# Kernel optimization log

Hardware: AMD Instinct MI355X
Metric: run time of the kernel (lower is better)

## Reference

```python
import jax, jax.numpy as jnp
import numpy as np

B, T, D = 1, 2048, 2048
H, HD = 16, 128          # n_heads, head_dim
RD = 64                  # rotary_emb_dim
K = 4                    # short conv kernel size
EPS = 1e-5


def setup_inputs() -> dict:
    key = jax.random.key(0)
    ks = jax.random.split(key, 10)
    hidden_states = jax.random.normal(ks[0], (B, T, D), dtype=jnp.float32)
    # standard RoPE tables for the rotary sub-dimension
    inv_freq = 1.0 / (10000.0 ** (jnp.arange(0, RD, 2, dtype=jnp.float32) / RD))  # [RD/2]
    pos = jnp.arange(T, dtype=jnp.float32)
    freqs = pos[:, None] * inv_freq[None, :]          # [T, RD/2]
    emb = jnp.concatenate([freqs, freqs], axis=-1)    # [T, RD]
    cos = jnp.broadcast_to(jnp.cos(emb)[None], (B, T, RD))
    sin = jnp.broadcast_to(jnp.sin(emb)[None], (B, T, RD))
    s = 1.0 / np.sqrt(D)
    return {
        "hidden_states": hidden_states,
        "cos": cos, "sin": sin,
        "Wq": jax.random.normal(ks[1], (D, D), jnp.float32) * s,
        "Wk": jax.random.normal(ks[2], (D, D), jnp.float32) * s,
        "Wv": jax.random.normal(ks[3], (D, D), jnp.float32) * s,
        "Wo": jax.random.normal(ks[4], (D, D), jnp.float32) * s,
        "conv_q_w": jax.random.normal(ks[5], (D, K), jnp.float32) * 0.5,
        "conv_k_w": jax.random.normal(ks[6], (D, K), jnp.float32) * 0.5,
        "conv_v_w": jax.random.normal(ks[7], (D, K), jnp.float32) * 0.5,
        "q_norm_w": jnp.ones((HD,), jnp.float32),
        "k_norm_w": jnp.ones((HD,), jnp.float32),
    }


def _causal_conv_silu(x, w):
    # x: [B,T,D], w: [D,K]; depthwise causal conv (tap K-1 hits current pos) + SiLU
    xp = jnp.pad(x, ((0, 0), (K - 1, 0), (0, 0)))
    y = sum(xp[:, j:j + T, :] * w[None, None, :, j] for j in range(K))
    return jax.nn.silu(y)


def _rms_norm(x, w):
    # x: [..., HD]
    var = jnp.mean(x * x, axis=-1, keepdims=True)
    return x * jax.lax.rsqrt(var + EPS) * w


def _rotate_half(x):
    x1, x2 = x[..., : x.shape[-1] // 2], x[..., x.shape[-1] // 2:]
    return jnp.concatenate([-x2, x1], axis=-1)


def _apply_rope(x, cos, sin):
    # x: [B,H,T,HD]; cos/sin: [B,T,RD] -> unsqueeze head dim; partial rotary branch
    cos = cos[:, None, :, :]
    sin = sin[:, None, :, :]
    x_rot, x_pass = x[..., :RD], x[..., RD:]
    x_rot = x_rot * cos + _rotate_half(x_rot) * sin
    # faithful to source: negates rotated part when rotary_dim != head_dim
    return jnp.concatenate([-x_rot, x_pass], axis=-1)


def reference(hidden_states, cos, sin, Wq, Wk, Wv, Wo,
              conv_q_w, conv_k_w, conv_v_w, q_norm_w, k_norm_w):
    # projections (Linear with bias=False: y = x @ W^T)
    q = hidden_states @ Wq.T
    k = hidden_states @ Wk.T
    v = hidden_states @ Wv.T
    # short causal depthwise conv + SiLU
    q = _causal_conv_silu(q, conv_q_w)
    k = _causal_conv_silu(k, conv_k_w)
    v = _causal_conv_silu(v, conv_v_w)
    # split heads: [B,T,D] -> [B,T,H,HD]
    q = q.reshape(B, T, H, HD)
    k = k.reshape(B, T, H, HD)
    v = v.reshape(B, T, H, HD)
    # per-head RMSNorm, then [B,H,T,HD]
    q = _rms_norm(q, q_norm_w).transpose(0, 2, 1, 3)
    k = _rms_norm(k, k_norm_w).transpose(0, 2, 1, 3)
    v = v.transpose(0, 2, 1, 3)
    # RoPE (partial)
    q = _apply_rope(q, cos, sin)
    k = _apply_rope(k, cos, sin)
    # causal attention
    scale = 1.0 / np.sqrt(HD)
    scores = jnp.einsum('bhqd,bhkd->bhqk', q, k) * scale
    causal = jnp.tril(jnp.ones((T, T), dtype=bool))
    scores = jnp.where(causal[None, None], scores, jnp.float32(-1e30))
    probs = jax.nn.softmax(scores, axis=-1)
    attn = jnp.einsum('bhqk,bhkd->bhqd', probs, v)
    # [B,H,T,HD] -> [B,T,D], output projection
    out = attn.transpose(0, 2, 1, 3).reshape(B, T, D) @ Wo.T
    return out
```

## Files before the change

### kernel.cpp

```cpp
#include <hip/hip_runtime.h>
#include <hip/hip_bf16.h>

#define T_SEQ 2048
#define D_MODEL 2048
#define NH 16
#define HDIM 128
#define RD_ROT 64

typedef __bf16 bf16x8 __attribute__((ext_vector_type(8)));
typedef float f32x4 __attribute__((ext_vector_type(4)));

__device__ __forceinline__ void async_copy16(const __bf16* g, __bf16* l) {
    __builtin_amdgcn_global_load_lds(
        (const __attribute__((address_space(1))) void*)g,
        (__attribute__((address_space(3))) void*)l, 16, 0, 0);
}

__global__ __launch_bounds__(256) void cast_kernel(
    const float* __restrict__ s0, const float* __restrict__ s1, const float* __restrict__ s2,
    const float* __restrict__ s3, const float* __restrict__ s4,
    __bf16* __restrict__ d0, __bf16* __restrict__ d1, __bf16* __restrict__ d2,
    __bf16* __restrict__ d3, __bf16* __restrict__ d4)
{
    const float* s; __bf16* d;
    switch (blockIdx.y) {
        case 0: s = s0; d = d0; break;
        case 1: s = s1; d = d1; break;
        case 2: s = s2; d = d2; break;
        case 3: s = s3; d = d3; break;
        default: s = s4; d = d4; break;
    }
    size_t base = (size_t)blockIdx.x * D_MODEL + (size_t)threadIdx.x * 8;
    f32x4 a = *(const f32x4*)(s + base);
    f32x4 b = *(const f32x4*)(s + base + 4);
    bf16x8 o;
    #pragma unroll
    for (int i = 0; i < 4; i++) { o[i] = (__bf16)a[i]; o[i + 4] = (__bf16)b[i]; }
    *(bf16x8*)(d + base) = o;
}

__global__ __launch_bounds__(256) void gemm_bt_kernel(
    const __bf16* __restrict__ A,
    const __bf16* __restrict__ B0, const __bf16* __restrict__ B1, const __bf16* __restrict__ B2,
    __bf16* __restrict__ C0, __bf16* __restrict__ C1, __bf16* __restrict__ C2)
{
    constexpr int BM = 128, BK = 32, KD = D_MODEL;
    const __bf16* Bm = blockIdx.z == 0 ? B0 : (blockIdx.z == 1 ? B1 : B2);
    __bf16* Cm       = blockIdx.z == 0 ? C0 : (blockIdx.z == 1 ? C1 : C2);

    __shared__ __align__(16) __bf16 As[BM * BK];
    __shared__ __align__(16) __bf16 Bs[BM * BK];

    const int lane = threadIdx.x & 63;
    const int wave = threadIdx.x >> 6;
    const int r15  = lane & 15;
    const int quad = lane >> 4;
    const int bm = blockIdx.x * BM;
    const int bn = blockIdx.y * BM;
    const int wm = (wave >> 1) * 64;
    const int wn = (wave & 1) * 64;

    f32x4 acc[4][4] = {};

    const int srow = wave * 32 + (lane >> 2);
    const int sg   = (lane & 3) ^ ((lane >> 2) & 3);

    for (int k0 = 0; k0 < KD; k0 += BK) {
        async_copy16(A  + (size_t)(bm + srow)      * KD + k0 + sg * 8, &As[wave * 1024]);
        async_copy16(A  + (size_t)(bm + srow + 16) * KD + k0 + sg * 8, &As[wave * 1024 + 512]);
        async_copy16(Bm + (size_t)(bn + srow)      * KD + k0 + sg * 8, &Bs[wave * 1024]);
        async_copy16(Bm + (size_t)(bn + srow + 16) * KD + k0 + sg * 8, &Bs[wave * 1024 + 512]);
        __syncthreads();

        bf16x8 av[4], bv[4];
        #pragma unroll
        for (int mt = 0; mt < 4; mt++)
            av[mt] = *(const bf16x8*)&As[(wm + mt * 16 + r15) * 32 + ((quad ^ (r15 & 3)) << 3)];
        #pragma unroll
        for (int nt = 0; nt < 4; nt++)
            bv[nt] = *(const bf16x8*)&Bs[(wn + nt * 16 + r15) * 32 + ((quad ^ (r15 & 3)) << 3)];
        #pragma unroll
        for (int mt = 0; mt < 4; mt++)
            #pragma unroll
            for (int nt = 0; nt < 4; nt++)
                acc[mt][nt] = __builtin_amdgcn_mfma_f32_16x16x32_bf16(av[mt], bv[nt], acc[mt][nt], 0, 0, 0);
        __syncthreads();
    }

    #pragma unroll
    for (int mt = 0; mt < 4; mt++) {
        #pragma unroll
        for (int r = 0; r < 4; r++) {
            size_t row = bm + wm + mt * 16 + quad * 4 + r;
            #pragma unroll
            for (int nt = 0; nt < 4; nt++) {
                size_t col = bn + wn + nt * 16 + r15;
                Cm[row * D_MODEL + col] = (__bf16)acc[mt][nt][r];
            }
        }
    }
}

__global__ __launch_bounds__(256) void gemm_bt_splitk_kernel(
    const __bf16* __restrict__ A, const __bf16* __restrict__ Bm, float* __restrict__ C)
{
    constexpr int BM = 128, BK = 32, KD = D_MODEL;
    __shared__ __align__(16) __bf16 As[BM * BK];
    __shared__ __align__(16) __bf16 Bs[BM * BK];

    const int lane = threadIdx.x & 63;
    const int wave = threadIdx.x >> 6;
    const int r15  = lane & 15;
    const int quad = lane >> 4;
    const int bm = blockIdx.x * BM;
    const int bn = blockIdx.y * BM;
    const int wm = (wave >> 1) * 64;
    const int wn = (wave & 1) * 64;
    const int kbase = blockIdx.z * (KD / 2);

    f32x4 acc[4][4] = {};
    const int srow = wave * 32 + (lane >> 2);
    const int sg   = (lane & 3) ^ ((lane >> 2) & 3);

    for (int k0 = kbase; k0 < kbase + KD / 2; k0 += BK) {
        async_copy16(A  + (size_t)(bm + srow)      * KD + k0 + sg * 8, &As[wave * 1024]);
        async_copy16(A  + (size_t)(bm + srow + 16) * KD + k0 + sg * 8, &As[wave * 1024 + 512]);
        async_copy16(Bm + (size_t)(bn + srow)      * KD + k0 + sg * 8, &Bs[wave * 1024]);
        async_copy16(Bm + (size_t)(bn + srow + 16) * KD + k0 + sg * 8, &Bs[wave * 1024 + 512]);
        __syncthreads();

        bf16x8 av[4], bv[4];
        #pragma unroll
        for (int mt = 0; mt < 4; mt++)
            av[mt] = *(const bf16x8*)&As[(wm + mt * 16 + r15) * 32 + ((quad ^ (r15 & 3)) << 3)];
        #pragma unroll
        for (int nt = 0; nt < 4; nt++)
            bv[nt] = *(const bf16x8*)&Bs[(wn + nt * 16 + r15) * 32 + ((quad ^ (r15 & 3)) << 3)];
        #pragma unroll
        for (int mt = 0; mt < 4; mt++)
            #pragma unroll
            for (int nt = 0; nt < 4; nt++)
                acc[mt][nt] = __builtin_amdgcn_mfma_f32_16x16x32_bf16(av[mt], bv[nt], acc[mt][nt], 0, 0, 0);
        __syncthreads();
    }

    #pragma unroll
    for (int mt = 0; mt < 4; mt++) {
        #pragma unroll
        for (int r = 0; r < 4; r++) {
            size_t row = bm + wm + mt * 16 + quad * 4 + r;
            #pragma unroll
            for (int nt = 0; nt < 4; nt++) {
                size_t col = bn + wn + nt * 16 + r15;
                atomicAdd(&C[row * D_MODEL + col], acc[mt][nt][r]);
            }
        }
    }
}

__global__ __launch_bounds__(256) void preproc_qk_kernel(
    const __bf16* __restrict__ q_raw, const __bf16* __restrict__ k_raw,
    const float* __restrict__ cwq, const float* __restrict__ cwk,
    const float* __restrict__ qnw, const float* __restrict__ knw,
    const float* __restrict__ cosb, const float* __restrict__ sinb,
    __bf16* __restrict__ q_proc, __bf16* __restrict__ k_proc)
{
    const int t = blockIdx.x;
    const int which = blockIdx.y;
    const __bf16* X = which ? k_raw : q_raw;
    const float*  W = which ? cwk : cwq;
    const float*  nw = which ? knw : qnw;
    __bf16* P = which ? k_proc : q_proc;
    const float SC = which ? 1.0f : 0.08838834764831845f;

    const int tid = threadIdx.x;
    const int c0  = tid * 8;
    const int h   = tid >> 4;
    const int dl0 = (tid & 15) * 8;

    f32x4 wv[8];
    #pragma unroll
    for (int i = 0; i < 8; i++) wv[i] = *(const f32x4*)&W[(c0 + i) * 4];

    float acc[8] = {};
    #pragma unroll
    for (int j = 0; j < 4; j++) {
        int tt = t + j - 3;
        if (tt >= 0) {
            bf16x8 xv = *(const bf16x8*)&X[(size_t)tt * D_MODEL + c0];
            #pragma unroll
            for (int i = 0; i < 8; i++) acc[i] += (float)xv[i] * wv[i][j];
        }
    }
    float sil[8], ss = 0.f;
    #pragma unroll
    for (int i = 0; i < 8; i++) {
        float s = acc[i] / (1.f + __expf(-acc[i]));
        sil[i] = s; ss += s * s;
    }
    #pragma unroll
    for (int off = 1; off < 16; off <<= 1) ss += __shfl_xor(ss, off);
    float inv = rsqrtf(ss * (1.f / 128.f) + 1e-5f);

    f32x4 nv0 = *(const f32x4*)&nw[dl0];
    f32x4 nv1 = *(const f32x4*)&nw[dl0 + 4];
    float yn[8];
    #pragma unroll
    for (int i = 0; i < 8; i++) yn[i] = sil[i] * inv * (i < 4 ? nv0[i] : nv1[i - 4]);

    float partner[8];
    #pragma unroll
    for (int i = 0; i < 8; i++) partner[i] = __shfl_xor(yn[i], 4);

    bf16x8 o;
    if (dl0 < RD_ROT) {
        f32x4 cv0 = *(const f32x4*)&cosb[t * RD_ROT + dl0];
        f32x4 cv1 = *(const f32x4*)&cosb[t * RD_ROT + dl0 + 4];
        f32x4 sv0 = *(const f32x4*)&sinb[t * RD_ROT + dl0];
        f32x4 sv1 = *(const f32x4*)&sinb[t * RD_ROT + dl0 + 4];
        #pragma unroll
        for (int i = 0; i < 8; i++) {
            int dl = dl0 + i;
            float c = i < 4 ? cv0[i] : cv1[i - 4];
            float s = i < 4 ? sv0[i] : sv1[i - 4];
            float rot = (dl < 32) ? -partner[i] : partner[i];
            o[i] = (__bf16)((yn[i] * c + rot * s) * SC);
        }
    } else {
        #pragma unroll
        for (int i = 0; i < 8; i++) o[i] = (__bf16)(yn[i] * SC);
    }
    *(bf16x8*)&P[((size_t)h * T_SEQ + t) * HDIM + dl0] = o;
}

__global__ __launch_bounds__(128) void preproc_v_kernel(
    const __bf16* __restrict__ v_raw, const float* __restrict__ cwv,
    __bf16* __restrict__ v_t)
{
    const int t0 = blockIdx.x * 8;
    const int h = blockIdx.y;
    const int dl = threadIdx.x;
    const int d = h * HDIM + dl;

    f32x4 wv = *(const f32x4*)&cwv[d * 4];
    float x[11];
    #pragma unroll
    for (int m = 0; m < 11; m++) {
        int tt = t0 - 3 + m;
        x[m] = (tt >= 0) ? (float)v_raw[(size_t)tt * D_MODEL + d] : 0.f;
    }
    bf16x8 o;
    #pragma unroll
    for (int r = 0; r < 8; r++) {
        float y = x[r] * wv[0] + x[r + 1] * wv[1] + x[r + 2] * wv[2] + x[r + 3] * wv[3];
        o[r] = (__bf16)(y / (1.f + __expf(-y)));
    }
    *(bf16x8*)&v_t[((size_t)h * HDIM + dl) * T_SEQ + t0] = o;
}

__global__ __launch_bounds__(256, 2) void attn_kernel(
    const __bf16* __restrict__ Qp,
    const __bf16* __restrict__ Kp,
    const __bf16* __restrict__ Vt,
    __bf16* __restrict__ Op)
{
    constexpr int TK = 64, PSTR = 72;
    __shared__ __align__(16) __bf16 Ks[2][TK * HDIM];
    __shared__ __align__(16) __bf16 Vs[2][HDIM * TK];
    __shared__ __align__(16) __bf16 Ps[64 * PSTR];

    const int lane = threadIdx.x & 63;
    const int wave = threadIdx.x >> 6;
    const int r15  = lane & 15;
    const int quad = lane >> 4;
    const int h = blockIdx.y;
    const int qi = (blockIdx.y & 8) ? ((int)gridDim.x - 1 - (int)blockIdx.x) : (int)blockIdx.x;
    const int q0 = qi * TK;

    const __bf16* Kb = Kp + (size_t)h * T_SEQ * HDIM;
    const __bf16* Vb = Vt + (size_t)h * HDIM * T_SEQ;

    const int kchunk = wave * 4;
    const int krow_l = (lane >> 4);
    const int kg     = lane & 15;
    const int vrow_l = (lane >> 3);
    const int vg     = lane & 7;

    bf16x8 qf[4];
    const __bf16* qbase = Qp + ((size_t)h * T_SEQ + q0 + wave * 16 + r15) * HDIM;
    #pragma unroll
    for (int s = 0; s < 4; s++) qf[s] = *(const bf16x8*)(qbase + s * 32 + quad * 8);

    f32x4 oacc[8] = {};
    float mrow[4], lsum[4];
    #pragma unroll
    for (int r = 0; r < 4; r++) { mrow[r] = -1e30f; lsum[r] = 0.f; }

    const int ntk = qi + 1;

    #pragma unroll
    for (int i = 0; i < 4; i++) {
        int ck = kchunk + i;
        int krow = ck * 4 + krow_l;
        int vrow = ck * 8 + vrow_l;
        async_copy16(Kb + (size_t)krow * HDIM + (kg ^ (krow & 15)) * 8, &Ks[0][ck * 512]);
        async_copy16(Vb + (size_t)vrow * T_SEQ + (vg ^ (vrow & 7)) * 8, &Vs[0][ck * 512]);
    }

    for (int it = 0; it < ntk; it++) {
        const int buf = it & 1;
        const bool last = (it == ntk - 1);
        __syncthreads();

        if (!last) {
            const int tkn = (it + 1) * TK;
            const int nbuf = buf ^ 1;
            #pragma unroll
            for (int i = 0; i < 4; i++) {
                int ck = kchunk + i;
                int krow = ck * 4 + krow_l;
                int vrow = ck * 8 + vrow_l;
                async_copy16(Kb + (size_t)(tkn + krow) * HDIM + (kg ^ (krow & 15)) * 8, &Ks[nbuf][ck * 512]);
                async_copy16(Vb + (size_t)vrow * T_SEQ + tkn + (vg ^ (vrow & 7)) * 8, &Vs[nbuf][ck * 512]);
            }
        }

        f32x4 sacc[4] = {};
        #pragma unroll
        for (int s = 0; s < 4; s++) {
            #pragma unroll
            for (int nt = 0; nt < 4; nt++) {
                bf16x8 kf = *(const bf16x8*)&Ks[buf][(nt * 16 + r15) * HDIM + (((s * 4 + quad) ^ r15) << 3)];
                sacc[nt] = __builtin_amdgcn_mfma_f32_16x16x32_bf16(qf[s], kf, sacc[nt], 0, 0, 0);
            }
        }

        float alpha[4];
        #pragma unroll
        for (int r = 0; r < 4; r++) {
            if (last) {
                int qrow = q0 + wave * 16 + quad * 4 + r;
                #pragma unroll
                for (int nt = 0; nt < 4; nt++) {
                    int kcol = it * TK + nt * 16 + r15;
                    if (kcol > qrow) sacc[nt][r] = -1e30f;
                }
            }
            float tm = fmaxf(fmaxf(sacc[0][r], sacc[1][r]), fmaxf(sacc[2][r], sacc[3][r]));
            #pragma unroll
            for (int off = 1; off < 16; off <<= 1) tm = fmaxf(tm, __shfl_xor(tm, off));
            float mn = fmaxf(mrow[r], tm);
            float a = __expf(mrow[r] - mn);
            mrow[r] = mn;
            alpha[r] = a;
            float ps = 0.f;
            #pragma unroll
            for (int nt = 0; nt < 4; nt++) {
                float p = __expf(sacc[nt][r] - mn);
                sacc[nt][r] = p;
                ps += p;
            }
            lsum[r] = lsum[r] * a + ps;
        }
        #pragma unroll
        for (int nt = 0; nt < 8; nt++)
            #pragma unroll
            for (int r = 0; r < 4; r++) oacc[nt][r] *= alpha[r];

        #pragma unroll
        for (int nt = 0; nt < 4; nt++)
            #pragma unroll
            for (int r = 0; r < 4; r++)
                Ps[(wave * 16 + quad * 4 + r) * PSTR + nt * 16 + r15] = (__bf16)sacc[nt][r];

        #pragma unroll
        for (int s2 = 0; s2 < 2; s2++) {
            bf16x8 pf = *(const bf16x8*)&Ps[(wave * 16 + r15) * PSTR + s2 * 32 + quad * 8];
            #pragma unroll
            for (int nt = 0; nt < 8; nt++) {
                bf16x8 vf = *(const bf16x8*)&Vs[buf][(nt * 16 + r15) * TK + (((s2 * 4 + quad) ^ (r15 & 7)) << 3)];
                oacc[nt] = __builtin_amdgcn_mfma_f32_16x16x32_bf16(pf, vf, oacc[nt], 0, 0, 0);
            }
        }
    }

    #pragma unroll
    for (int r = 0; r < 4; r++) {
        float l = lsum[r];
        #pragma unroll
        for (int off = 1; off < 16; off <<= 1) l += __shfl_xor(l, off);
        float inv = 1.0f / l;
        size_t row = q0 + wave * 16 + quad * 4 + r;
        #pragma unroll
        for (int nt = 0; nt < 8; nt++)
            Op[row * D_MODEL + h * HDIM + nt * 16 + r15] = (__bf16)(oacc[nt][r] * inv);
    }
}

extern "C" void kernel_launch(void* const* d_in, const int* in_sizes, int n_in,
                              void* d_out, int out_size, void* d_ws, size_t ws_size,
                              hipStream_t stream) {
    (void)in_sizes; (void)n_in; (void)out_size; (void)ws_size;
    const float* hidden = (const float*)d_in[0];
    const float* cosb   = (const float*)d_in[1];
    const float* sinb   = (const float*)d_in[2];
    const float* Wq     = (const float*)d_in[3];
    const float* Wk     = (const float*)d_in[4];
    const float* Wv     = (const float*)d_in[5];
    const float* Wo     = (const float*)d_in[6];
    const float* cwq    = (const float*)d_in[7];
    const float* cwk    = (const float*)d_in[8];
    const float* cwv    = (const float*)d_in[9];
    const float* qnw    = (const float*)d_in[10];
    const float* knw    = (const float*)d_in[11];

    const size_t NEL = (size_t)T_SEQ * D_MODEL;
    __bf16* ws = (__bf16*)d_ws;
    __bf16* h_bf   = ws + 0 * NEL;
    __bf16* Wq_bf  = ws + 1 * NEL;
    __bf16* Wk_bf  = ws + 2 * NEL;
    __bf16* Wv_bf  = ws + 3 * NEL;
    __bf16* Wo_bf  = ws + 4 * NEL;
    __bf16* q_raw  = ws + 5 * NEL;
    __bf16* k_raw  = ws + 6 * NEL;
    __bf16* v_raw  = ws + 7 * NEL;
    __bf16* q_proc = Wq_bf;
    __bf16* k_proc = Wk_bf;
    __bf16* v_t    = Wv_bf;
    __bf16* attn_b = h_bf;
    float*  out    = (float*)d_out;

    cast_kernel<<<dim3(T_SEQ, 5), 256, 0, stream>>>(hidden, Wq, Wk, Wv, Wo,
                                                    h_bf, Wq_bf, Wk_bf, Wv_bf, Wo_bf);
    gemm_bt_kernel<<<dim3(16, 16, 3), 256, 0, stream>>>(
        h_bf, Wq_bf, Wk_bf, Wv_bf, q_raw, k_raw, v_raw);
    preproc_qk_kernel<<<dim3(T_SEQ, 2), 256, 0, stream>>>(
        q_raw, k_raw, cwq, cwk, qnw, knw, cosb, sinb, q_proc, k_proc);
    preproc_v_kernel<<<dim3(T_SEQ / 8, NH), 128, 0, stream>>>(v_raw, cwv, v_t);
    attn_kernel<<<dim3(T_SEQ / 64, NH), 256, 0, stream>>>(q_proc, k_proc, v_t, attn_b);
    hipMemsetAsync(d_out, 0, NEL * sizeof(float), stream);
    gemm_bt_splitk_kernel<<<dim3(16, 16, 2), 256, 0, stream>>>(attn_b, Wo_bf, out);
}
```

Baseline: 345.2 us.

## Rework attention to 32x32 MFMA with split-K waves and max-free softmax

Result: slower. 354.8 us (+2.8%).

```diff
diff --git a/kernel.cpp b/kernel.cpp
--- a/kernel.cpp
+++ b/kernel.cpp
@@ -9,6 +9,7 @@
 
 typedef __bf16 bf16x8 __attribute__((ext_vector_type(8)));
 typedef float f32x4 __attribute__((ext_vector_type(4)));
+typedef float f32x16 __attribute__((ext_vector_type(16)));
 
 __device__ __forceinline__ void async_copy16(const __bf16* g, __bf16* l) {
     __builtin_amdgcn_global_load_lds(
@@ -264,37 +265,42 @@
     const __bf16* __restrict__ Vt,
     __bf16* __restrict__ Op)
 {
-    constexpr int TK = 64, PSTR = 72;
+    constexpr int TK = 64;
     __shared__ __align__(16) __bf16 Ks[2][TK * HDIM];
     __shared__ __align__(16) __bf16 Vs[2][HDIM * TK];
-    __shared__ __align__(16) __bf16 Ps[64 * PSTR];
+    __shared__ __align__(16) __bf16 Ps[4][32 * 64];
+    float* Omrg = (float*)Ks;
+    float* Lmrg = (float*)Ps;
 
     const int lane = threadIdx.x & 63;
     const int wave = threadIdx.x >> 6;
-    const int r15  = lane & 15;
-    const int quad = lane >> 4;
+    const int rowg = wave >> 1;
+    const int par  = wave & 1;
+    const int c31  = lane & 31;
+    const int h5   = lane >> 5;
     const int h = blockIdx.y;
     const int qi = (blockIdx.y & 8) ? ((int)gridDim.x - 1 - (int)blockIdx.x) : (int)blockIdx.x;
-    const int q0 = qi * TK;
+    const int q0 = qi * 64;
+    const int rw = q0 + rowg * 32;
 
     const __bf16* Kb = Kp + (size_t)h * T_SEQ * HDIM;
     const __bf16* Vb = Vt + (size_t)h * HDIM * T_SEQ;
 
+    bf16x8 qf[8];
+    {
+        const __bf16* qb = Qp + ((size_t)h * T_SEQ + rw + c31) * HDIM + h5 * 8;
+        #pragma unroll
+        for (int kc = 0; kc < 8; kc++) qf[kc] = *(const bf16x8*)(qb + kc * 16);
+    }
+
     const int kchunk = wave * 4;
-    const int krow_l = (lane >> 4);
+    const int krow_l = lane >> 4;
     const int kg     = lane & 15;
-    const int vrow_l = (lane >> 3);
+    const int vrow_l = lane >> 3;
     const int vg     = lane & 7;
 
-    bf16x8 qf[4];
-    const __bf16* qbase = Qp + ((size_t)h * T_SEQ + q0 + wave * 16 + r15) * HDIM;
-    #pragma unroll
-    for (int s = 0; s < 4; s++) qf[s] = *(const bf16x8*)(qbase + s * 32 + quad * 8);
-
-    f32x4 oacc[8] = {};
-    float mrow[4], lsum[4];
-    #pragma unroll
-    for (int r = 0; r < 4; r++) { mrow[r] = -1e30f; lsum[r] = 0.f; }
+    f32x16 oacc[4] = {};
+    float lsum[16] = {};
 
     const int ntk = qi + 1;
 
@@ -309,10 +315,9 @@
 
     for (int it = 0; it < ntk; it++) {
         const int buf = it & 1;
-        const bool last = (it == ntk - 1);
         __syncthreads();
 
-        if (!last) {
+        if (it + 1 < ntk) {
             const int tkn = (it + 1) * TK;
             const int nbuf = buf ^ 1;
             #pragma unroll
@@ -325,75 +330,99 @@
             }
         }
 
-        f32x4 sacc[4] = {};
-        #pragma unroll
-        for (int s = 0; s < 4; s++) {
+        if ((it & 1) != par) continue;
+        const bool diag = (it == qi);
+        const int ntmax = (diag && rowg == 0) ? 1 : 2;
+
+        f32x16 sacc[2] = {};
+        #pragma unroll
+        for (int nt = 0; nt < 2; nt++) {
+            if (nt >= ntmax) break;
+            #pragma unroll
+            for (int kc = 0; kc < 8; kc++) {
+                int row = nt * 32 + c31;
+                int g = kc * 2 + h5;
+                bf16x8 kf = *(const bf16x8*)&Ks[buf][row * HDIM + ((g ^ (row & 15)) << 3)];
+                sacc[nt] = __builtin_amdgcn_mfma_f32_32x32x16_bf16(qf[kc], kf, sacc[nt], 0, 0, 0);
+            }
+        }
+
+        #pragma unroll
+        for (int nt = 0; nt < 2; nt++) {
+            if (nt >= ntmax) break;
+            const bool dmask = diag && (nt == rowg);
+            int col = it * TK + nt * 32 + c31;
+            #pragma unroll
+            for (int reg = 0; reg < 16; reg++) {
+                int row = rw + (reg & 3) + 8 * (reg >> 2) + 4 * h5;
+                float p = __expf(sacc[nt][reg]);
+                if (dmask && col > row) p = 0.f;
+                sacc[nt][reg] = p;
+                lsum[reg] += p;
+            }
+        }
+
+        #pragma unroll
+        for (int nt = 0; nt < 2; nt++) {
+            if (nt >= ntmax) break;
+            int col = nt * 32 + c31;
+            int g = col >> 3;
+            #pragma unroll
+            for (int reg = 0; reg < 16; reg++) {
+                int rl = (reg & 3) + 8 * (reg >> 2) + 4 * h5;
+                Ps[wave][rl * 64 + (((g ^ (rl & 7)) << 3) | (col & 7))] = (__bf16)sacc[nt][reg];
+            }
+        }
+        const int kcmax = (diag && rowg == 0) ? 2 : 4;
+
+        #pragma unroll
+        for (int kc = 0; kc < 4; kc++) {
+            if (kc >= kcmax) break;
+            int gp = kc * 2 + h5;
+            bf16x8 pf = *(const bf16x8*)&Ps[wave][c31 * 64 + ((gp ^ (c31 & 7)) << 3)];
             #pragma unroll
             for (int nt = 0; nt < 4; nt++) {
-                bf16x8 kf = *(const bf16x8*)&Ks[buf][(nt * 16 + r15) * HDIM + (((s * 4 + quad) ^ r15) << 3)];
-                sacc[nt] = __builtin_amdgcn_mfma_f32_16x16x32_bf16(qf[s], kf, sacc[nt], 0, 0, 0);
-            }
-        }
-
-        float alpha[4];
-        #pragma unroll
-        for (int r = 0; r < 4; r++) {
-            if (last) {
-                int qrow = q0 + wave * 16 + quad * 4 + r;
-                #pragma unroll
-                for (int nt = 0; nt < 4; nt++) {
-                    int kcol = it * TK + nt * 16 + r15;
-                    if (kcol > qrow) sacc[nt][r] = -1e30f;
-                }
-            }
-            float tm = fmaxf(fmaxf(sacc[0][r], sacc[1][r]), fmaxf(sacc[2][r], sacc[3][r]));
-            #pragma unroll
-            for (int off = 1; off < 16; off <<= 1) tm = fmaxf(tm, __shfl_xor(tm, off));
-            float mn = fmaxf(mrow[r], tm);
-            float a = __expf(mrow[r] - mn);
-            mrow[r] = mn;
-            alpha[r] = a;
-            float ps = 0.f;
-            #pragma unroll
-            for (int nt = 0; nt < 4; nt++) {
-                float p = __expf(sacc[nt][r] - mn);
-                sacc[nt][r] = p;
-                ps += p;
-            }
-            lsum[r] = lsum[r] * a + ps;
-        }
-        #pragma unroll
-        for (int nt = 0; nt < 8; nt++)
-            #pragma unroll
-            for (int r = 0; r < 4; r++) oacc[nt][r] *= alpha[r];
-
+                int vrow = nt * 32 + c31;
+                int gv = kc * 2 + h5;
+                bf16x8 vf = *(const bf16x8*)&Vs[buf][vrow * TK + ((gv ^ (vrow & 7)) << 3)];
+                oacc[nt] = __builtin_amdgcn_mfma_f32_32x32x16_bf16(pf, vf, oacc[nt], 0, 0, 0);
+            }
+        }
+    }
+
+    __syncthreads();
+    if (par == 1) {
         #pragma unroll
         for (int nt = 0; nt < 4; nt++)
             #pragma unroll
-            for (int r = 0; r < 4; r++)
-                Ps[(wave * 16 + quad * 4 + r) * PSTR + nt * 16 + r15] = (__bf16)sacc[nt][r];
-
-        #pragma unroll
-        for (int s2 = 0; s2 < 2; s2++) {
-            bf16x8 pf = *(const bf16x8*)&Ps[(wave * 16 + r15) * PSTR + s2 * 32 + quad * 8];
-            #pragma unroll
-            for (int nt = 0; nt < 8; nt++) {
-                bf16x8 vf = *(const bf16x8*)&Vs[buf][(nt * 16 + r15) * TK + (((s2 * 4 + quad) ^ (r15 & 7)) << 3)];
-                oacc[nt] = __builtin_amdgcn_mfma_f32_16x16x32_bf16(pf, vf, oacc[nt], 0, 0, 0);
-            }
-        }
-    }
-
-    #pragma unroll
-    for (int r = 0; r < 4; r++) {
-        float l = lsum[r];
-        #pragma unroll
-        for (int off = 1; off < 16; off <<= 1) l += __shfl_xor(l, off);
-        float inv = 1.0f / l;
-        size_t row = q0 + wave * 16 + quad * 4 + r;
-        #pragma unroll
-        for (int nt = 0; nt < 8; nt++)
-            Op[row * D_MODEL + h * HDIM + nt * 16 + r15] = (__bf16)(oacc[nt][r] * inv);
+            for (int reg = 0; reg < 16; reg++)
+                Omrg[rowg * 4096 + lane * 64 + nt * 16 + reg] = oacc[nt][reg];
+        #pragma unroll
+        for (int reg = 0; reg < 16; reg++)
+            Lmrg[rowg * 1024 + lane * 16 + reg] = lsum[reg];
+    }
+    __syncthreads();
+    if (par == 0) {
+        #pragma unroll
+        for (int nt = 0; nt < 4; nt++)
+            #pragma unroll
+            for (int reg = 0; reg < 16; reg++)
+                oacc[nt][reg] += Omrg[rowg * 4096 + lane * 64 + nt * 16 + reg];
+        float linv[16];
+        #pragma unroll
+        for (int reg = 0; reg < 16; reg++) {
+            float l = lsum[reg] + Lmrg[rowg * 1024 + lane * 16 + reg];
+            #pragma unroll
+            for (int off = 1; off < 32; off <<= 1) l += __shfl_xor(l, off);
+            linv[reg] = 1.0f / l;
+        }
+        #pragma unroll
+        for (int reg = 0; reg < 16; reg++) {
+            size_t row = rw + (reg & 3) + 8 * (reg >> 2) + 4 * h5;
+            #pragma unroll
+            for (int nt = 0; nt < 4; nt++)
+                Op[row * D_MODEL + h * HDIM + nt * 32 + c31] = (__bf16)(oacc[nt][reg] * linv[reg]);
+        }
     }
 }
 
```
